# Performance work log

Hardware: AMD Instinct MI355X
Metric: run time of the kernel (lower is better)

Reference implementation:

```python
import jax, jax.numpy as jnp
import numpy as np

DIM = 1024
HEADS = 16
HEAD_DIM = DIM // HEADS
SCALE = HEAD_DIM ** -0.5


def setup_inputs() -> dict:
    key = jax.random.key(0)
    ks = jax.random.split(key, 9)
    b, n, m = 4, 1024, 1024
    x = jax.random.normal(ks[0], (b, n, DIM), dtype=jnp.float32)
    context = jax.random.normal(ks[1], (b, m, DIM), dtype=jnp.float32)
    mask = jax.random.randint(ks[2], (b, n, 32, 32), 0, 2, dtype=jnp.int32)
    s = DIM ** -0.5
    Wq = jax.random.normal(ks[3], (DIM, DIM), dtype=jnp.float32) * s
    bq = jnp.zeros((DIM,), dtype=jnp.float32)
    Wkv = jax.random.normal(ks[4], (DIM, 2 * DIM), dtype=jnp.float32) * s
    bkv = jnp.zeros((2 * DIM,), dtype=jnp.float32)
    Wp = jax.random.normal(ks[5], (DIM, DIM), dtype=jnp.float32) * s
    bp = jnp.zeros((DIM,), dtype=jnp.float32)
    return {"x": x, "context": context, "mask": mask,
            "Wq": Wq, "bq": bq, "Wkv": Wkv, "bkv": bkv, "Wp": Wp, "bp": bp}


def reference(x, context, mask, Wq, bq, Wkv, bkv, Wp, bp):
    b, n, _ = x.shape
    m = context.shape[1]
    h, d = HEADS, HEAD_DIM
    # projections
    q = (x @ Wq + bq).reshape(b, n, h, d).transpose(0, 2, 1, 3)       # [b,h,n,d]
    kv = (context @ Wkv + bkv).reshape(b, m, 2, h, d)
    k = kv[:, :, 0].transpose(0, 2, 1, 3)                              # [b,h,m,d]
    v = kv[:, :, 1].transpose(0, 2, 1, 3)                              # [b,h,m,d]
    dots = jnp.einsum('bhnd,bhmd->bhnm', q, k) * SCALE                 # [b,h,n,m]
    # mask: [b,n,H,W] -> [b,1,n,m]; masked_fill where mask == 0
    mflat = mask.reshape(b, n, m)[:, None]                             # [b,1,n,m]
    dots = jnp.where(mflat == 0, -jnp.inf, dots)
    attn = jax.nn.softmax(dots, axis=-1)
    out = jnp.einsum('bhnm,bhmd->bhnd', attn, v)
    out = out.transpose(0, 2, 1, 3).reshape(b, n, h * d)
    return out @ Wp + bp
```

## Files before the change

kernel.cpp:

```cpp
#include <hip/hip_runtime.h>

typedef __bf16 bf16;
typedef __bf16 bf16x8 __attribute__((ext_vector_type(8)));
typedef __bf16 bf16x4 __attribute__((ext_vector_type(4)));
typedef float f32x4 __attribute__((ext_vector_type(4)));
typedef unsigned long long u64;

#define MFMA16(a, b, c) __builtin_amdgcn_mfma_f32_16x16x32_bf16(a, b, c, 0, 0, 0)

__device__ __forceinline__ void gl_lds16(const void* g, void* l) {
  __builtin_amdgcn_global_load_lds(
      (const __attribute__((address_space(1))) unsigned int*)g,
      (__attribute__((address_space(3))) unsigned int*)l, 16, 0, 0);
}

__global__ __launch_bounds__(256)
void prep_k(const float* __restrict__ Wq, const float* __restrict__ Wkv,
            const float* __restrict__ Wp, const int* __restrict__ mask,
            const float* __restrict__ context, const float* __restrict__ x,
            bf16* __restrict__ BqkvT, bf16* __restrict__ WpT,
            u64* __restrict__ maskbits, bf16* __restrict__ cb,
            bf16* __restrict__ xb) {
  const int bx = blockIdx.x;
  const int tid = threadIdx.x;
  if (bx >= 3328) {
    const size_t i = ((size_t)(bx - 3328) * 256 + tid) * 8;
    f32x4 a0 = *(const f32x4*)(x + i);
    f32x4 a1 = *(const f32x4*)(x + i + 4);
    bf16x8 t;
#pragma unroll
    for (int j = 0; j < 4; ++j) { t[j] = (bf16)a0[j]; t[4 + j] = (bf16)a1[j]; }
    *(bf16x8*)(xb + i) = t;
    return;
  }
  if (bx >= 1280) {
    const size_t i = ((size_t)(bx - 1280) * 256 + tid) * 8;
    f32x4 a0 = *(const f32x4*)(context + i);
    f32x4 a1 = *(const f32x4*)(context + i + 4);
    bf16x8 t;
#pragma unroll
    for (int j = 0; j < 4; ++j) { t[j] = (bf16)a0[j]; t[4 + j] = (bf16)a1[j]; }
    *(bf16x8*)(cb + i) = t;
    return;
  }
  if (bx >= 1024) {
    const int idx = (bx - 1024) * 256 + tid;
    const int4* p = (const int4*)(mask + (size_t)idx * 64);
    u64 v = 0;
#pragma unroll
    for (int i = 0; i < 16; ++i) {
      int4 m = p[i];
      v |= (u64)(m.x != 0) << (4 * i);
      v |= (u64)(m.y != 0) << (4 * i + 1);
      v |= (u64)(m.z != 0) << (4 * i + 2);
      v |= (u64)(m.w != 0) << (4 * i + 3);
    }
    maskbits[idx] = v;
    return;
  }
  const int ct = bx >> 4, rt = bx & 15;
  const float* src;
  bf16* dst;
  int C, c0, drow0;
  if (ct < 16) {
    src = Wq; C = 1024; c0 = ct * 64; dst = BqkvT; drow0 = c0;
  } else if (ct < 48) {
    src = Wkv; C = 2048; c0 = (ct - 16) * 64; dst = BqkvT; drow0 = 1024 + c0;
  } else {
    src = Wp; C = 1024; c0 = (ct - 48) * 64; dst = WpT; drow0 = c0;
  }
  __shared__ bf16 T[64][72];
  const int r0 = rt * 64;
#pragma unroll
  for (int i = 0; i < 2; ++i) {
    int c = i * 256 + tid;
    int row = c >> 3, col = (c & 7) * 8;
    const float* sp = &src[(size_t)(r0 + row) * C + c0 + col];
    f32x4 a0 = *(const f32x4*)sp;
    f32x4 a1 = *(const f32x4*)(sp + 4);
    bf16x8 t;
#pragma unroll
    for (int j = 0; j < 4; ++j) { t[j] = (bf16)a0[j]; t[4 + j] = (bf16)a1[j]; }
    *(bf16x8*)&T[row][col] = t;
  }
  __syncthreads();
#pragma unroll
  for (int i = 0; i < 2; ++i) {
    int c = i * 256 + tid;
    int orow = c >> 3, ocol = (c & 7) * 8;
    bf16x8 v;
#pragma unroll
    for (int j = 0; j < 8; ++j) v[j] = T[ocol + j][orow];
    *(bf16x8*)&dst[(size_t)(drow0 + orow) * 1024 + r0 + ocol] = v;
  }
}

template <int EPI, int BN>
__global__ __launch_bounds__(256, 3)
void gemm_db2(const bf16* __restrict__ A0, const bf16* __restrict__ A1,
              const bf16* __restrict__ Bt, const float* __restrict__ bias0,
              const float* __restrict__ bias1, bf16* __restrict__ oq,
              bf16* __restrict__ ok, bf16* __restrict__ ovt,
              float* __restrict__ outf) {
  constexpr int NJ = BN / 32;
  __shared__ bf16 As[2][128][32];
  __shared__ bf16 Bs[2][BN][32];
  const int tid = threadIdx.x;
  const int lane = tid & 63;
  const int w = tid >> 6;
  const int wm = (w >> 1) * 64;
  const int wn = (w & 1) * (BN / 2);
  const int l15 = lane & 15, l4 = lane >> 4;
  const int lrow = lane >> 2;
  const int lcg = (lane & 3) ^ ((lrow >> 1) & 3);
  const int rdc = (l4 ^ ((l15 >> 1) & 3)) * 8;
  const int m0 = blockIdx.x * 128;
  const int n0 = blockIdx.y * BN;

  const bf16* Asrc = (EPI == 1) ? ((n0 < 1024) ? A0 : A1) : A0;

  f32x4 acc[4][NJ] = {};

#define STAGE(kk, buf)                                                        \
  {                                                                           \
    _Pragma("unroll") for (int it = 0; it < 2; ++it) {                        \
      const int r = w * 32 + it * 16;                                         \
      gl_lds16(&Asrc[(size_t)(m0 + r + lrow) * 1024 + (kk) + lcg * 8],        \
               &As[buf][r][0]);                                               \
    }                                                                         \
    _Pragma("unroll") for (int it = 0; it < BN / 64; ++it) {                  \
      const int r = w * (BN / 4) + it * 16;                                   \
      gl_lds16(&Bt[(size_t)(n0 + r + lrow) * 1024 + (kk) + lcg * 8],          \
               &Bs[buf][r][0]);                                               \
    }                                                                         \
  }

#define COMPUTE(buf)                                                          \
  {                                                                           \
    bf16x8 af[4], bfr[NJ];                                                    \
    _Pragma("unroll") for (int i = 0; i < 4; ++i) af[i] =                     \
        *(const bf16x8*)&As[buf][wm + i * 16 + l15][rdc];                     \
    _Pragma("unroll") for (int j = 0; j < NJ; ++j) bfr[j] =                   \
        *(const bf16x8*)&Bs[buf][wn + j * 16 + l15][rdc];                     \
    _Pragma("unroll") for (int i = 0; i < 4; ++i)                             \
        _Pragma("unroll") for (int j = 0; j < NJ; ++j) acc[i][j] =            \
            MFMA16(af[i], bfr[j], acc[i][j]);                                 \
  }

  STAGE(0, 0);
  for (int k = 0; k < 32; k += 2) {
    __syncthreads();
    STAGE((k + 1) * 32, 1);
    COMPUTE(0);
    __syncthreads();
    if (k < 30) STAGE((k + 2) * 32, 0);
    COMPUTE(1);
  }
#undef STAGE
#undef COMPUTE

  const float SCALE2 = 0.18033688011112042f;
#pragma unroll
  for (int j = 0; j < NJ; ++j) {
    const int col = n0 + wn + j * 16 + l15;
    float bc;
    if (EPI == 1) bc = (col < 1024) ? bias0[col] : bias1[col - 1024];
    else bc = bias0[col];
#pragma unroll
    for (int i = 0; i < 4; ++i) {
#pragma unroll
      for (int r = 0; r < 4; ++r) {
        const int row = m0 + wm + i * 16 + l4 * 4 + r;
        const float v = acc[i][j][r] + bc;
        if (EPI == 0) {
          outf[(size_t)row * 1024 + col] = v;
        } else {
          const int b = row >> 10, n = row & 1023;
          if (col < 1024) {
            const int h = col >> 6, d = col & 63;
            oq[(((size_t)(b * 16 + h)) * 1024 + n) * 64 + d] =
                (bf16)(v * SCALE2);
          } else {
            const int ckv = col - 1024;
            const int s = ckv >> 10, c2 = ckv & 1023;
            const int h = c2 >> 6, d = c2 & 63;
            if (s == 0)
              ok[(((size_t)(b * 16 + h)) * 1024 + n) * 64 + d] = (bf16)v;
            else
              ovt[(((size_t)(b * 16 + h)) * 64 + d) * 1024 + n] = (bf16)v;
          }
        }
      }
    }
  }
}

__global__ __launch_bounds__(256, 4)
void attn_kernel(const bf16* __restrict__ q, const bf16* __restrict__ k,
                 const bf16* __restrict__ vT, const u64* __restrict__ maskbits,
                 bf16* __restrict__ ao) {
  const int bh = blockIdx.x;
  const int ntile = blockIdx.y;
  const int b = bh >> 4, h = bh & 15;
  const int tid = threadIdx.x;
  const int lane = tid & 63;
  const int w = tid >> 6;
  const int l15 = lane & 15, l4 = lane >> 4;

  __shared__ bf16 Ks[2][64][64];
  __shared__ bf16 Vts[2][64][64];
  __shared__ bf16 Pw[4][16][64];

  const size_t base = (size_t)bh * 65536;
  const int nrow0 = ntile * 64 + w * 16;

  bf16x8 qf[2];
#pragma unroll
  for (int ks = 0; ks < 2; ++ks)
    qf[ks] = *(const bf16x8*)&q[base + (size_t)(nrow0 + l15) * 64 + ks * 32 +
                                l4 * 8];

  const u64* mb = maskbits + (size_t)(b * 1024 + nrow0 + l15) * 16;

  const int srow = lane >> 3;
  const int sgl = (lane & 7) ^ srow;
  const bf16* kp = &k[base + (size_t)(w * 16 + srow) * 64 + sgl * 8];
  const bf16* vp = &vT[base + (size_t)(w * 16 + srow) * 1024 + sgl * 8];

  const int rc0 = ((0 + l4) ^ (l15 & 7)) * 8;
  const int rc1 = ((4 + l4) ^ (l15 & 7)) * 8;

  f32x4 o[4] = {};
  float lsum = 0.0f;

#define STAGEA(mt_, buf_)                                                     \
  {                                                                           \
    _Pragma("unroll") for (int it = 0; it < 2; ++it) {                        \
      gl_lds16(kp + (size_t)((mt_)*64 + it * 8) * 64,                         \
               &Ks[buf_][w * 16 + it * 8][0]);                                \
      gl_lds16(vp + (size_t)(it * 8) * 1024 + (mt_)*64,                       \
               &Vts[buf_][w * 16 + it * 8][0]);                               \
    }                                                                         \
  }

  STAGEA(0, 0);
  for (int mt = 0; mt < 16; ++mt) {
    const int cur = mt & 1;
    __syncthreads();
    if (mt < 15) STAGEA(mt + 1, cur ^ 1);
    const u64 wmt = mb[mt];

    f32x4 s[4];
#pragma unroll
    for (int sub = 0; sub < 4; ++sub)
      s[sub] = f32x4{-12.f, -12.f, -12.f, -12.f};
    __builtin_amdgcn_s_setprio(1);
#pragma unroll
    for (int sub = 0; sub < 4; ++sub) {
      bf16x8 kf0 = *(const bf16x8*)&Ks[cur][sub * 16 + l15][rc0];
      bf16x8 kf1 = *(const bf16x8*)&Ks[cur][sub * 16 + l15][rc1];
      s[sub] = MFMA16(kf0, qf[0], s[sub]);
      s[sub] = MFMA16(kf1, qf[1], s[sub]);
    }
    __builtin_amdgcn_s_setprio(0);

#pragma unroll
    for (int sub = 0; sub < 4; ++sub) {
      const int kbit = sub * 16 + l4 * 4;
      float p[4];
#pragma unroll
      for (int r = 0; r < 4; ++r) {
        float e = exp2f(s[sub][r]);
        p[r] = ((wmt >> (kbit + r)) & 1) ? e : 0.0f;
      }
      lsum += (p[0] + p[1]) + (p[2] + p[3]);
      bf16x4 pv;
#pragma unroll
      for (int r = 0; r < 4; ++r) pv[r] = (bf16)p[r];
      const int gw = sub * 2 + (l4 >> 1);
      char* pd = (char*)&Pw[w][l15][0] + ((gw ^ (l15 & 7)) * 16 + (l4 & 1) * 8);
      *(bf16x4*)pd = pv;
    }

    bf16x8 af0 = *(const bf16x8*)&Pw[w][l15][rc0];
    bf16x8 af1 = *(const bf16x8*)&Pw[w][l15][rc1];
    __builtin_amdgcn_s_setprio(1);
#pragma unroll
    for (int sub = 0; sub < 4; ++sub) {
      bf16x8 vf0 = *(const bf16x8*)&Vts[cur][sub * 16 + l15][rc0];
      bf16x8 vf1 = *(const bf16x8*)&Vts[cur][sub * 16 + l15][rc1];
      o[sub] = MFMA16(af0, vf0, o[sub]);
      o[sub] = MFMA16(af1, vf1, o[sub]);
    }
    __builtin_amdgcn_s_setprio(0);
  }
#undef STAGEA

  float t = lsum;
  t += __shfl_xor(t, 16);
  t += __shfl_xor(t, 32);
  float inv[4];
#pragma unroll
  for (int r = 0; r < 4; ++r) inv[r] = 1.0f / __shfl(t, l4 * 4 + r);

#pragma unroll
  for (int sub = 0; sub < 4; ++sub) {
#pragma unroll
    for (int r = 0; r < 4; ++r) {
      const int n = nrow0 + l4 * 4 + r;
      const size_t idx =
          ((size_t)(b * 1024 + n)) * 1024 + h * 64 + sub * 16 + l15;
      ao[idx] = (bf16)(o[sub][r] * inv[r]);
    }
  }
}

extern "C" void kernel_launch(void* const* d_in, const int* in_sizes, int n_in,
                              void* d_out, int out_size, void* d_ws,
                              size_t ws_size, hipStream_t stream) {
  const float* x = (const float*)d_in[0];
  const float* context = (const float*)d_in[1];
  const int* mask = (const int*)d_in[2];
  const float* Wq = (const float*)d_in[3];
  const float* bq = (const float*)d_in[4];
  const float* Wkv = (const float*)d_in[5];
  const float* bkv = (const float*)d_in[6];
  const float* Wp = (const float*)d_in[7];
  const float* bp = (const float*)d_in[8];
  float* out = (float*)d_out;

  char* ws = (char*)d_ws;
  bf16* cb = (bf16*)(ws);
  bf16* aow = (bf16*)(ws);
  bf16* xb = (bf16*)(ws + (8ull << 20));
  bf16* BqkvT = (bf16*)(ws + (16ull << 20));
  bf16* qw = (bf16*)(ws + (22ull << 20));
  bf16* kw = (bf16*)(ws + (30ull << 20));
  bf16* vtw = (bf16*)(ws + (38ull << 20));
  u64* maskbits = (u64*)(ws + (46ull << 20));
  bf16* WpT = (bf16*)(ws + (46ull << 20) + (512ull << 10));

  const dim3 blk(256);

  prep_k<<<dim3(5376), blk, 0, stream>>>(Wq, Wkv, Wp, mask, context, x, BqkvT,
                                         WpT, maskbits, cb, xb);

  gemm_db2<1, 128><<<dim3(32, 24), blk, 0, stream>>>(xb, cb, BqkvT, bq, bkv,
                                                     qw, kw, vtw, nullptr);

  attn_kernel<<<dim3(64, 16), blk, 0, stream>>>(qw, kw, vtw, maskbits, aow);

  gemm_db2<0, 64><<<dim3(32, 16), blk, 0, stream>>>(aow, nullptr, WpT, bp,
                                                    nullptr, nullptr, nullptr,
                                                    nullptr, out);
}
```

Baseline: 211.6 us.

## Triple-buffer GEMM LDS pipeline with vmcnt waits and a single barrier per step

Replaces the double-buffered GEMM main loop with a three-stage LDS ring. Each step now uses one barrier plus an explicit s_waitcnt vmcnt, so two tiles of global-to-LDS loads can be in flight while one tile is being computed, and the per-step barrier count drops from two to one. Bias loads are hoisted ahead of the main loop, and the launch-bounds occupancy hint for the BN=64 case is raised to 4. Shared memory per block grows by one stage, which may reduce occupancy. Correctness also depends on the hand-counted vmcnt values matching the number of loads issued per stage.

```diff
diff --git a/kernel.cpp b/kernel.cpp
--- a/kernel.cpp
+++ b/kernel.cpp
@@ -12,6 +12,17 @@
   __builtin_amdgcn_global_load_lds(
       (const __attribute__((address_space(1))) unsigned int*)g,
       (__attribute__((address_space(3))) unsigned int*)l, 16, 0, 0);
+}
+
+template <int N>
+__device__ __forceinline__ void wait_vmcnt() {
+  asm volatile("s_waitcnt vmcnt(%0)" ::"n"(N) : "memory");
+}
+
+__device__ __forceinline__ void bar() {
+  asm volatile("" ::: "memory");
+  __builtin_amdgcn_s_barrier();
+  asm volatile("" ::: "memory");
 }
 
 __global__ __launch_bounds__(256)
@@ -96,15 +107,16 @@
 }
 
 template <int EPI, int BN>
-__global__ __launch_bounds__(256, 3)
-void gemm_db2(const bf16* __restrict__ A0, const bf16* __restrict__ A1,
-              const bf16* __restrict__ Bt, const float* __restrict__ bias0,
-              const float* __restrict__ bias1, bf16* __restrict__ oq,
-              bf16* __restrict__ ok, bf16* __restrict__ ovt,
-              float* __restrict__ outf) {
+__global__ __launch_bounds__(256, BN == 128 ? 3 : 4)
+void gemm_p3(const bf16* __restrict__ A0, const bf16* __restrict__ A1,
+             const bf16* __restrict__ Bt, const float* __restrict__ bias0,
+             const float* __restrict__ bias1, bf16* __restrict__ oq,
+             bf16* __restrict__ ok, bf16* __restrict__ ovt,
+             float* __restrict__ outf) {
   constexpr int NJ = BN / 32;
-  __shared__ bf16 As[2][128][32];
-  __shared__ bf16 Bs[2][BN][32];
+  constexpr int S = 2 + BN / 64;
+  __shared__ bf16 As[3][128][32];
+  __shared__ bf16 Bs[3][BN][32];
   const int tid = threadIdx.x;
   const int lane = tid & 63;
   const int w = tid >> 6;
@@ -118,6 +130,14 @@
   const int n0 = blockIdx.y * BN;
 
   const bf16* Asrc = (EPI == 1) ? ((n0 < 1024) ? A0 : A1) : A0;
+
+  float bc[NJ];
+#pragma unroll
+  for (int j = 0; j < NJ; ++j) {
+    const int col = n0 + wn + j * 16 + l15;
+    if (EPI == 1) bc[j] = (col < 1024) ? bias0[col] : bias1[col - 1024];
+    else bc[j] = bias0[col];
+  }
 
   f32x4 acc[4][NJ] = {};
 
@@ -148,14 +168,20 @@
   }
 
   STAGE(0, 0);
-  for (int k = 0; k < 32; k += 2) {
-    __syncthreads();
-    STAGE((k + 1) * 32, 1);
-    COMPUTE(0);
-    __syncthreads();
-    if (k < 30) STAGE((k + 2) * 32, 0);
-    COMPUTE(1);
-  }
+  STAGE(32, 1);
+#pragma unroll 3
+  for (int k = 0; k < 30; ++k) {
+    wait_vmcnt<S>();
+    bar();
+    STAGE((k + 2) * 32, (k + 2) % 3);
+    COMPUTE(k % 3);
+  }
+  wait_vmcnt<S>();
+  bar();
+  COMPUTE(0);
+  wait_vmcnt<0>();
+  bar();
+  COMPUTE(1);
 #undef STAGE
 #undef COMPUTE
 
@@ -163,15 +189,12 @@
 #pragma unroll
   for (int j = 0; j < NJ; ++j) {
     const int col = n0 + wn + j * 16 + l15;
-    float bc;
-    if (EPI == 1) bc = (col < 1024) ? bias0[col] : bias1[col - 1024];
-    else bc = bias0[col];
 #pragma unroll
     for (int i = 0; i < 4; ++i) {
 #pragma unroll
       for (int r = 0; r < 4; ++r) {
         const int row = m0 + wm + i * 16 + l4 * 4 + r;
-        const float v = acc[i][j][r] + bc;
+        const float v = acc[i][j][r] + bc[j];
         if (EPI == 0) {
           outf[(size_t)row * 1024 + col] = v;
         } else {
@@ -345,12 +368,12 @@
   prep_k<<<dim3(5376), blk, 0, stream>>>(Wq, Wkv, Wp, mask, context, x, BqkvT,
                                          WpT, maskbits, cb, xb);
 
-  gemm_db2<1, 128><<<dim3(32, 24), blk, 0, stream>>>(xb, cb, BqkvT, bq, bkv,
-                                                     qw, kw, vtw, nullptr);
+  gemm_p3<1, 128><<<dim3(32, 24), blk, 0, stream>>>(xb, cb, BqkvT, bq, bkv,
+                                                    qw, kw, vtw, nullptr);
 
   attn_kernel<<<dim3(64, 16), blk, 0, stream>>>(qw, kw, vtw, maskbits, aow);
 
-  gemm_db2<0, 64><<<dim3(32, 16), blk, 0, stream>>>(aow, nullptr, WpT, bp,
-                                                    nullptr, nullptr, nullptr,
-                                                    nullptr, out);
-}
+  gemm_p3<0, 64><<<dim3(32, 16), blk, 0, stream>>>(aow, nullptr, WpT, bp,
+                                                   nullptr, nullptr, nullptr,
+                                                   nullptr, out);
+}
```

After: 209.3 us. Within noise of the previous version (-1.1%).

## Fuse pipeline into one cooperative persistent kernel with grid syncs

Applied to the files above, without the earlier changes.

Merges the prep, QKV GEMM, attention and output-projection stages into a single cooperative kernel of 768 blocks separated by grid-wide barriers, with a fallback to separate launches if the cooperative launch fails. The goal is to remove per-kernel launch gaps and tail effects. Attention is also changed so each wave handles 32 query rows instead of 16, reusing each K/V LDS fragment across two row tiles with half as many blocks. In exchange, grid syncs and fence overhead are added, the attention and final GEMM stages use only 512 of the 768 blocks, and register pressure rises.

```diff
diff --git a/kernel.cpp b/kernel.cpp
--- a/kernel.cpp
+++ b/kernel.cpp
@@ -1,4 +1,7 @@
 #include <hip/hip_runtime.h>
+#include <hip/hip_cooperative_groups.h>
+
+namespace cg = cooperative_groups;
 
 typedef __bf16 bf16;
 typedef __bf16 bf16x8 __attribute__((ext_vector_type(8)));
@@ -14,17 +17,16 @@
       (__attribute__((address_space(3))) unsigned int*)l, 16, 0, 0);
 }
 
-__global__ __launch_bounds__(256)
-void prep_k(const float* __restrict__ Wq, const float* __restrict__ Wkv,
-            const float* __restrict__ Wp, const int* __restrict__ mask,
-            const float* __restrict__ context, const float* __restrict__ x,
-            bf16* __restrict__ BqkvT, bf16* __restrict__ WpT,
-            u64* __restrict__ maskbits, bf16* __restrict__ cb,
-            bf16* __restrict__ xb) {
-  const int bx = blockIdx.x;
-  const int tid = threadIdx.x;
-  if (bx >= 3328) {
-    const size_t i = ((size_t)(bx - 3328) * 256 + tid) * 8;
+
+__device__ __forceinline__ void prep_unit(
+    char* smraw, int u, int tid, const float* __restrict__ Wq,
+    const float* __restrict__ Wkv, const float* __restrict__ Wp,
+    const int* __restrict__ mask, const float* __restrict__ context,
+    const float* __restrict__ x, bf16* __restrict__ BqkvT,
+    bf16* __restrict__ WpT, u64* __restrict__ maskbits, bf16* __restrict__ cb,
+    bf16* __restrict__ xb) {
+  if (u >= 3328) {
+    const size_t i = ((size_t)(u - 3328) * 256 + tid) * 8;
     f32x4 a0 = *(const f32x4*)(x + i);
     f32x4 a1 = *(const f32x4*)(x + i + 4);
     bf16x8 t;
@@ -33,8 +35,8 @@
     *(bf16x8*)(xb + i) = t;
     return;
   }
-  if (bx >= 1280) {
-    const size_t i = ((size_t)(bx - 1280) * 256 + tid) * 8;
+  if (u >= 1280) {
+    const size_t i = ((size_t)(u - 1280) * 256 + tid) * 8;
     f32x4 a0 = *(const f32x4*)(context + i);
     f32x4 a1 = *(const f32x4*)(context + i + 4);
     bf16x8 t;
@@ -43,8 +45,8 @@
     *(bf16x8*)(cb + i) = t;
     return;
   }
-  if (bx >= 1024) {
-    const int idx = (bx - 1024) * 256 + tid;
+  if (u >= 1024) {
+    const int idx = (u - 1024) * 256 + tid;
     const int4* p = (const int4*)(mask + (size_t)idx * 64);
     u64 v = 0;
 #pragma unroll
@@ -58,7 +60,8 @@
     maskbits[idx] = v;
     return;
   }
-  const int ct = bx >> 4, rt = bx & 15;
+  auto T = reinterpret_cast<bf16(*)[72]>(smraw);
+  const int ct = u >> 4, rt = u & 15;
   const float* src;
   bf16* dst;
   int C, c0, drow0;
@@ -69,7 +72,6 @@
   } else {
     src = Wp; C = 1024; c0 = (ct - 48) * 64; dst = WpT; drow0 = c0;
   }
-  __shared__ bf16 T[64][72];
   const int r0 = rt * 64;
 #pragma unroll
   for (int i = 0; i < 2; ++i) {
@@ -93,18 +95,19 @@
     for (int j = 0; j < 8; ++j) v[j] = T[ocol + j][orow];
     *(bf16x8*)&dst[(size_t)(drow0 + orow) * 1024 + r0 + ocol] = v;
   }
+  __syncthreads();
 }
 
 template <int EPI, int BN>
-__global__ __launch_bounds__(256, 3)
-void gemm_db2(const bf16* __restrict__ A0, const bf16* __restrict__ A1,
-              const bf16* __restrict__ Bt, const float* __restrict__ bias0,
-              const float* __restrict__ bias1, bf16* __restrict__ oq,
-              bf16* __restrict__ ok, bf16* __restrict__ ovt,
-              float* __restrict__ outf) {
+__device__ __forceinline__ void gemm_body(
+    char* smraw, int m0, int n0, const bf16* __restrict__ A0,
+    const bf16* __restrict__ A1, const bf16* __restrict__ Bt,
+    const float* __restrict__ bias0, const float* __restrict__ bias1,
+    bf16* __restrict__ oq, bf16* __restrict__ ok, bf16* __restrict__ ovt,
+    float* __restrict__ outf) {
   constexpr int NJ = BN / 32;
-  __shared__ bf16 As[2][128][32];
-  __shared__ bf16 Bs[2][BN][32];
+  auto As = reinterpret_cast<bf16(*)[128][32]>(smraw);
+  auto Bs = reinterpret_cast<bf16(*)[BN][32]>(smraw + 16384);
   const int tid = threadIdx.x;
   const int lane = tid & 63;
   const int w = tid >> 6;
@@ -114,8 +117,6 @@
   const int lrow = lane >> 2;
   const int lcg = (lane & 3) ^ ((lrow >> 1) & 3);
   const int rdc = (l4 ^ ((l15 >> 1) & 3)) * 8;
-  const int m0 = blockIdx.x * 128;
-  const int n0 = blockIdx.y * BN;
 
   const bf16* Asrc = (EPI == 1) ? ((n0 < 1024) ? A0 : A1) : A0;
 
@@ -195,30 +196,32 @@
   }
 }
 
-__global__ __launch_bounds__(256, 4)
-void attn_kernel(const bf16* __restrict__ q, const bf16* __restrict__ k,
-                 const bf16* __restrict__ vT, const u64* __restrict__ maskbits,
-                 bf16* __restrict__ ao) {
-  const int bh = blockIdx.x;
-  const int ntile = blockIdx.y;
+__device__ __forceinline__ void attn_body(char* smraw, int bh, int ntile,
+                                          const bf16* __restrict__ q,
+                                          const bf16* __restrict__ k,
+                                          const bf16* __restrict__ vT,
+                                          const u64* __restrict__ maskbits,
+                                          bf16* __restrict__ ao) {
+  auto Ks = reinterpret_cast<bf16(*)[64][64]>(smraw);
+  auto Vts = reinterpret_cast<bf16(*)[64][64]>(smraw + 16384);
+  auto Pw = reinterpret_cast<bf16(*)[32][64]>(smraw + 32768);
   const int b = bh >> 4, h = bh & 15;
   const int tid = threadIdx.x;
   const int lane = tid & 63;
   const int w = tid >> 6;
   const int l15 = lane & 15, l4 = lane >> 4;
 
-  __shared__ bf16 Ks[2][64][64];
-  __shared__ bf16 Vts[2][64][64];
-  __shared__ bf16 Pw[4][16][64];
-
   const size_t base = (size_t)bh * 65536;
-  const int nrow0 = ntile * 64 + w * 16;
-
-  bf16x8 qf[2];
-#pragma unroll
-  for (int ks = 0; ks < 2; ++ks)
-    qf[ks] = *(const bf16x8*)&q[base + (size_t)(nrow0 + l15) * 64 + ks * 32 +
-                                l4 * 8];
+  const int nrow0 = ntile * 128 + w * 32;
+
+  bf16x8 qf[2][2];
+#pragma unroll
+  for (int f = 0; f < 2; ++f)
+#pragma unroll
+    for (int ks = 0; ks < 2; ++ks)
+      qf[f][ks] = *(const bf16x8*)&q[base +
+                                     (size_t)(nrow0 + f * 16 + l15) * 64 +
+                                     ks * 32 + l4 * 8];
 
   const u64* mb = maskbits + (size_t)(b * 1024 + nrow0 + l15) * 16;
 
@@ -230,8 +233,8 @@
   const int rc0 = ((0 + l4) ^ (l15 & 7)) * 8;
   const int rc1 = ((4 + l4) ^ (l15 & 7)) * 8;
 
-  f32x4 o[4] = {};
-  float lsum = 0.0f;
+  f32x4 o[2][4] = {};
+  float lsum[2] = {0.0f, 0.0f};
 
 #define STAGEA(mt_, buf_)                                                     \
   {                                                                           \
@@ -248,71 +251,168 @@
     const int cur = mt & 1;
     __syncthreads();
     if (mt < 15) STAGEA(mt + 1, cur ^ 1);
-    const u64 wmt = mb[mt];
-
-    f32x4 s[4];
-#pragma unroll
-    for (int sub = 0; sub < 4; ++sub)
-      s[sub] = f32x4{-12.f, -12.f, -12.f, -12.f};
+    const u64 wm0 = mb[mt];
+    const u64 wm1 = mb[256 + mt];
+
+    f32x4 s[2][4];
+#pragma unroll
+    for (int f = 0; f < 2; ++f)
+#pragma unroll
+      for (int sub = 0; sub < 4; ++sub)
+        s[f][sub] = f32x4{-12.f, -12.f, -12.f, -12.f};
     __builtin_amdgcn_s_setprio(1);
 #pragma unroll
     for (int sub = 0; sub < 4; ++sub) {
       bf16x8 kf0 = *(const bf16x8*)&Ks[cur][sub * 16 + l15][rc0];
       bf16x8 kf1 = *(const bf16x8*)&Ks[cur][sub * 16 + l15][rc1];
-      s[sub] = MFMA16(kf0, qf[0], s[sub]);
-      s[sub] = MFMA16(kf1, qf[1], s[sub]);
+      s[0][sub] = MFMA16(kf0, qf[0][0], s[0][sub]);
+      s[0][sub] = MFMA16(kf1, qf[0][1], s[0][sub]);
+      s[1][sub] = MFMA16(kf0, qf[1][0], s[1][sub]);
+      s[1][sub] = MFMA16(kf1, qf[1][1], s[1][sub]);
     }
     __builtin_amdgcn_s_setprio(0);
 
 #pragma unroll
-    for (int sub = 0; sub < 4; ++sub) {
-      const int kbit = sub * 16 + l4 * 4;
-      float p[4];
-#pragma unroll
-      for (int r = 0; r < 4; ++r) {
-        float e = exp2f(s[sub][r]);
-        p[r] = ((wmt >> (kbit + r)) & 1) ? e : 0.0f;
+    for (int f = 0; f < 2; ++f) {
+      const u64 wmt = f ? wm1 : wm0;
+#pragma unroll
+      for (int sub = 0; sub < 4; ++sub) {
+        const int kbit = sub * 16 + l4 * 4;
+        float p[4];
+#pragma unroll
+        for (int r = 0; r < 4; ++r) {
+          float e = exp2f(s[f][sub][r]);
+          p[r] = ((wmt >> (kbit + r)) & 1) ? e : 0.0f;
+        }
+        lsum[f] += (p[0] + p[1]) + (p[2] + p[3]);
+        bf16x4 pv;
+#pragma unroll
+        for (int r = 0; r < 4; ++r) pv[r] = (bf16)p[r];
+        const int gw = sub * 2 + (l4 >> 1);
+        char* pd = (char*)&Pw[w][f * 16 + l15][0] +
+                   ((gw ^ (l15 & 7)) * 16 + (l4 & 1) * 8);
+        *(bf16x4*)pd = pv;
       }
-      lsum += (p[0] + p[1]) + (p[2] + p[3]);
-      bf16x4 pv;
-#pragma unroll
-      for (int r = 0; r < 4; ++r) pv[r] = (bf16)p[r];
-      const int gw = sub * 2 + (l4 >> 1);
-      char* pd = (char*)&Pw[w][l15][0] + ((gw ^ (l15 & 7)) * 16 + (l4 & 1) * 8);
-      *(bf16x4*)pd = pv;
-    }
-
-    bf16x8 af0 = *(const bf16x8*)&Pw[w][l15][rc0];
-    bf16x8 af1 = *(const bf16x8*)&Pw[w][l15][rc1];
+    }
+
+    bf16x8 af[2][2];
+#pragma unroll
+    for (int f = 0; f < 2; ++f) {
+      af[f][0] = *(const bf16x8*)&Pw[w][f * 16 + l15][rc0];
+      af[f][1] = *(const bf16x8*)&Pw[w][f * 16 + l15][rc1];
+    }
     __builtin_amdgcn_s_setprio(1);
 #pragma unroll
     for (int sub = 0; sub < 4; ++sub) {
       bf16x8 vf0 = *(const bf16x8*)&Vts[cur][sub * 16 + l15][rc0];
       bf16x8 vf1 = *(const bf16x8*)&Vts[cur][sub * 16 + l15][rc1];
-      o[sub] = MFMA16(af0, vf0, o[sub]);
-      o[sub] = MFMA16(af1, vf1, o[sub]);
+      o[0][sub] = MFMA16(af[0][0], vf0, o[0][sub]);
+      o[0][sub] = MFMA16(af[0][1], vf1, o[0][sub]);
+      o[1][sub] = MFMA16(af[1][0], vf0, o[1][sub]);
+      o[1][sub] = MFMA16(af[1][1], vf1, o[1][sub]);
     }
     __builtin_amdgcn_s_setprio(0);
   }
 #undef STAGEA
 
-  float t = lsum;
-  t += __shfl_xor(t, 16);
-  t += __shfl_xor(t, 32);
-  float inv[4];
-#pragma unroll
-  for (int r = 0; r < 4; ++r) inv[r] = 1.0f / __shfl(t, l4 * 4 + r);
-
-#pragma unroll
-  for (int sub = 0; sub < 4; ++sub) {
-#pragma unroll
-    for (int r = 0; r < 4; ++r) {
-      const int n = nrow0 + l4 * 4 + r;
-      const size_t idx =
-          ((size_t)(b * 1024 + n)) * 1024 + h * 64 + sub * 16 + l15;
-      ao[idx] = (bf16)(o[sub][r] * inv[r]);
-    }
-  }
+  float inv[2][4];
+#pragma unroll
+  for (int f = 0; f < 2; ++f) {
+    float t = lsum[f];
+    t += __shfl_xor(t, 16);
+    t += __shfl_xor(t, 32);
+#pragma unroll
+    for (int r = 0; r < 4; ++r) inv[f][r] = 1.0f / __shfl(t, l4 * 4 + r);
+  }
+
+#pragma unroll
+  for (int f = 0; f < 2; ++f) {
+#pragma unroll
+    for (int sub = 0; sub < 4; ++sub) {
+#pragma unroll
+      for (int r = 0; r < 4; ++r) {
+        const int n = nrow0 + f * 16 + l4 * 4 + r;
+        const size_t idx =
+            ((size_t)(b * 1024 + n)) * 1024 + h * 64 + sub * 16 + l15;
+        ao[idx] = (bf16)(o[f][sub][r] * inv[f][r]);
+      }
+    }
+  }
+}
+
+__global__ __launch_bounds__(256, 3)
+void mega(const float* __restrict__ x, const float* __restrict__ context,
+          const int* __restrict__ mask, const float* __restrict__ Wq,
+          const float* __restrict__ bq, const float* __restrict__ Wkv,
+          const float* __restrict__ bkv, const float* __restrict__ Wp,
+          const float* __restrict__ bp, float* __restrict__ out,
+          char* __restrict__ ws) {
+  __shared__ __align__(16) char smraw[49152];
+  bf16* cb = (bf16*)(ws);
+  bf16* aow = (bf16*)(ws);
+  bf16* xb = (bf16*)(ws + (8ull << 20));
+  bf16* BqkvT = (bf16*)(ws + (16ull << 20));
+  bf16* qw = (bf16*)(ws + (22ull << 20));
+  bf16* kw = (bf16*)(ws + (30ull << 20));
+  bf16* vtw = (bf16*)(ws + (38ull << 20));
+  u64* maskbits = (u64*)(ws + (46ull << 20));
+  bf16* WpT = (bf16*)(ws + (46ull << 20) + (512ull << 10));
+
+  cg::grid_group gg = cg::this_grid();
+  const int bid = blockIdx.x;
+  const int tid = threadIdx.x;
+
+#pragma unroll
+  for (int i = 0; i < 7; ++i)
+    prep_unit(smraw, bid + 768 * i, tid, Wq, Wkv, Wp, mask, context, x, BqkvT,
+              WpT, maskbits, cb, xb);
+  __threadfence();
+  gg.sync();
+
+  gemm_body<1, 128>(smraw, (bid & 31) * 128, (bid >> 5) * 128, xb, cb, BqkvT,
+                    bq, bkv, qw, kw, vtw, nullptr);
+  __threadfence();
+  gg.sync();
+
+  if (bid < 512) attn_body(smraw, bid & 63, bid >> 6, qw, kw, vtw, maskbits, aow);
+  __threadfence();
+  gg.sync();
+
+  if (bid < 512)
+    gemm_body<0, 64>(smraw, (bid & 31) * 128, (bid >> 5) * 64, aow, nullptr,
+                     WpT, bp, nullptr, nullptr, nullptr, nullptr, out);
+}
+
+__global__ __launch_bounds__(256)
+void prep_k(const float* __restrict__ Wq, const float* __restrict__ Wkv,
+            const float* __restrict__ Wp, const int* __restrict__ mask,
+            const float* __restrict__ context, const float* __restrict__ x,
+            bf16* __restrict__ BqkvT, bf16* __restrict__ WpT,
+            u64* __restrict__ maskbits, bf16* __restrict__ cb,
+            bf16* __restrict__ xb) {
+  __shared__ __align__(16) char smraw[9216];
+  prep_unit(smraw, blockIdx.x, threadIdx.x, Wq, Wkv, Wp, mask, context, x,
+            BqkvT, WpT, maskbits, cb, xb);
+}
+
+template <int EPI, int BN>
+__global__ __launch_bounds__(256, 3)
+void gemm_k(const bf16* __restrict__ A0, const bf16* __restrict__ A1,
+            const bf16* __restrict__ Bt, const float* __restrict__ bias0,
+            const float* __restrict__ bias1, bf16* __restrict__ oq,
+            bf16* __restrict__ ok, bf16* __restrict__ ovt,
+            float* __restrict__ outf) {
+  __shared__ __align__(16) char smraw[16384 + 2 * BN * 32 * 2];
+  gemm_body<EPI, BN>(smraw, blockIdx.x * 128, blockIdx.y * BN, A0, A1, Bt,
+                     bias0, bias1, oq, ok, ovt, outf);
+}
+
+__global__ __launch_bounds__(256, 2)
+void attn_k(const bf16* __restrict__ q, const bf16* __restrict__ k,
+            const bf16* __restrict__ vT, const u64* __restrict__ maskbits,
+            bf16* __restrict__ ao) {
+  __shared__ __align__(16) char smraw[49152];
+  attn_body(smraw, blockIdx.x, blockIdx.y, q, k, vT, maskbits, ao);
 }
 
 extern "C" void kernel_launch(void* const* d_in, const int* in_sizes, int n_in,
@@ -330,27 +430,31 @@
   float* out = (float*)d_out;
 
   char* ws = (char*)d_ws;
-  bf16* cb = (bf16*)(ws);
-  bf16* aow = (bf16*)(ws);
-  bf16* xb = (bf16*)(ws + (8ull << 20));
-  bf16* BqkvT = (bf16*)(ws + (16ull << 20));
-  bf16* qw = (bf16*)(ws + (22ull << 20));
-  bf16* kw = (bf16*)(ws + (30ull << 20));
-  bf16* vtw = (bf16*)(ws + (38ull << 20));
-  u64* maskbits = (u64*)(ws + (46ull << 20));
-  bf16* WpT = (bf16*)(ws + (46ull << 20) + (512ull << 10));
-
-  const dim3 blk(256);
-
-  prep_k<<<dim3(5376), blk, 0, stream>>>(Wq, Wkv, Wp, mask, context, x, BqkvT,
-                                         WpT, maskbits, cb, xb);
-
-  gemm_db2<1, 128><<<dim3(32, 24), blk, 0, stream>>>(xb, cb, BqkvT, bq, bkv,
+
+  void* margs[] = {(void*)&x,  (void*)&context, (void*)&mask, (void*)&Wq,
+                   (void*)&bq, (void*)&Wkv,     (void*)&bkv,  (void*)&Wp,
+                   (void*)&bp, (void*)&out,     (void*)&ws};
+  hipError_t err = hipLaunchCooperativeKernel((const void*)mega, dim3(768),
+                                              dim3(256), margs, 0, stream);
+  if (err != hipSuccess) {
+    (void)hipGetLastError();
+    bf16* cb = (bf16*)(ws);
+    bf16* aow = (bf16*)(ws);
+    bf16* xb = (bf16*)(ws + (8ull << 20));
+    bf16* BqkvT = (bf16*)(ws + (16ull << 20));
+    bf16* qw = (bf16*)(ws + (22ull << 20));
+    bf16* kw = (bf16*)(ws + (30ull << 20));
+    bf16* vtw = (bf16*)(ws + (38ull << 20));
+    u64* maskbits = (u64*)(ws + (46ull << 20));
+    bf16* WpT = (bf16*)(ws + (46ull << 20) + (512ull << 10));
+    const dim3 blk(256);
+    prep_k<<<dim3(5376), blk, 0, stream>>>(Wq, Wkv, Wp, mask, context, x,
+                                           BqkvT, WpT, maskbits, cb, xb);
+    gemm_k<1, 128><<<dim3(32, 24), blk, 0, stream>>>(xb, cb, BqkvT, bq, bkv,
                                                      qw, kw, vtw, nullptr);
-
-  attn_kernel<<<dim3(64, 16), blk, 0, stream>>>(qw, kw, vtw, maskbits, aow);
-
-  gemm_db2<0, 64><<<dim3(32, 16), blk, 0, stream>>>(aow, nullptr, WpT, bp,
+    attn_k<<<dim3(64, 8), blk, 0, stream>>>(qw, kw, vtw, maskbits, aow);
+    gemm_k<0, 64><<<dim3(32, 16), blk, 0, stream>>>(aow, nullptr, WpT, bp,
                                                     nullptr, nullptr, nullptr,
                                                     nullptr, out);
-}
+  }
+}
```

After: 830.7 us. 3.93x slower.
